# Kernel optimization log

Hardware: AMD Instinct MI355X
Metric: run time of the kernel (lower is better)

Reference implementation:

```python
import jax, jax.numpy as jnp
import numpy as np

DIM = 384
NUM_HEADS = 8
HEAD_DIM = DIM // NUM_HEADS
SCALE = HEAD_DIM ** -0.5
MLP_HIDDEN = int(DIM * 4.0)
EPS = 1e-6


def setup_inputs() -> dict:
    key = jax.random.key(0)
    ks = jax.random.split(key, 8)
    s = 0.02
    return {
        "x": jax.random.normal(ks[0], (2, DIM, 8, 16, 16), dtype=jnp.float32),
        "g1": jnp.ones((DIM,), jnp.float32),
        "b1": jnp.zeros((DIM,), jnp.float32),
        "Wqkv": jax.random.normal(ks[1], (DIM, 3 * DIM), jnp.float32) * s,  # no bias (qkv_bias=False)
        "Wo": jax.random.normal(ks[2], (DIM, DIM), jnp.float32) * s,
        "bo": jnp.zeros((DIM,), jnp.float32),
        "g2": jnp.ones((DIM,), jnp.float32),
        "b2": jnp.zeros((DIM,), jnp.float32),
        "W1": jax.random.normal(ks[3], (DIM, MLP_HIDDEN), jnp.float32) * s,
        "b1m": jnp.zeros((MLP_HIDDEN,), jnp.float32),
        "W2": jax.random.normal(ks[4], (MLP_HIDDEN, DIM), jnp.float32) * s,
        "b2m": jnp.zeros((DIM,), jnp.float32),
    }


def _layernorm(x, g, b):
    mu = jnp.mean(x, axis=-1, keepdims=True)
    var = jnp.mean(jnp.square(x - mu), axis=-1, keepdims=True)
    return (x - mu) * jax.lax.rsqrt(var + EPS) * g + b


def _attention(h, Wqkv, Wo, bo):
    B, N, C = h.shape
    qkv = h @ Wqkv  # [B, N, 3C]
    qkv = qkv.reshape(B, N, 3, NUM_HEADS, HEAD_DIM).transpose(2, 0, 3, 1, 4)
    q, k, v = qkv[0], qkv[1], qkv[2]  # each [B, H, N, d]
    att = jax.nn.softmax(jnp.einsum('bhxd,bhyd->bhxy', q, k) * SCALE, axis=-1)
    out = jnp.einsum('bhxy,bhyd->bhxd', att, v)  # [B, H, N, d]
    out = out.transpose(0, 2, 1, 3).reshape(B, N, C)
    return out @ Wo + bo


def reference(x, g1, b1, Wqkv, Wo, bo, g2, b2, W1, b1m, W2, b2m):
    B, C, D, H, W = x.shape
    h = x.transpose(0, 2, 3, 4, 1).reshape(B, D * H * W, C)  # b (d h w) c
    h = h + _attention(_layernorm(h, g1, b1), Wqkv, Wo, bo)
    m = _layernorm(h, g2, b2)
    m = jax.nn.gelu(m @ W1 + b1m, approximate=False) @ W2 + b2m
    h = h + m
    return h.reshape(B, D, H, W, C).transpose(0, 4, 1, 2, 3)
```

## Files before the change

kernel.cpp:

```cpp
#include <hip/hip_runtime.h>
#include <hip/hip_bf16.h>
#include <math.h>

#define DIM    384
#define NHEAD  8
#define HDIM   48
#define NTOK   2048
#define BATCH  2
#define TOKS   (BATCH * NTOK)
#define HIDDEN 1536

typedef __bf16 bf16x8 __attribute__((ext_vector_type(8)));
typedef float  f32x4  __attribute__((ext_vector_type(4)));
typedef unsigned short u16;

union bfu { __hip_bfloat16 h; u16 u; };

__device__ __forceinline__ void load_lds16(const void* g, void* l) {
    __builtin_amdgcn_global_load_lds(
        (const __attribute__((address_space(1))) void*)g,
        (__attribute__((address_space(3))) void*)l, 16, 0, 0);
}

__global__ __launch_bounds__(256) void prep(
    const float* __restrict__ Wqkv, __hip_bfloat16* __restrict__ WqkvT,
    const float* __restrict__ x, const float* __restrict__ g,
    const float* __restrict__ bta,
    float* __restrict__ hOut, __hip_bfloat16* __restrict__ y) {
    __shared__ __align__(16) char smem[384 * 33 * 4];
    int id = blockIdx.x;
    int tid = threadIdx.x;
    if (id < 432) {
        float (*t)[33] = (float(*)[33])smem;
        const int R = 384, C = 1152, tc = C / 32;
        int i0 = (id / tc) * 32, j0 = (id % tc) * 32;
        int tx = tid & 31, ty = tid >> 5;
#pragma unroll
        for (int k = 0; k < 32; k += 8)
            t[ty + k][tx] = Wqkv[(size_t)(i0 + ty + k) * C + j0 + tx];
        __syncthreads();
#pragma unroll
        for (int k = 0; k < 32; k += 8)
            WqkvT[(size_t)(j0 + ty + k) * R + i0 + tx] = __float2bfloat16(t[tx][ty + k]);
    } else {
        float* t = (float*)smem;
        int id2 = id - 432;
        int n0 = (id2 & 63) * 32, b = id2 >> 6;
        const float* xb = x + (size_t)b * DIM * NTOK;
        for (int idx = tid; idx < 384 * 32; idx += 256) {
            int c = idx >> 5, n = idx & 31;
            t[c * 33 + n] = xb[(size_t)c * NTOK + n0 + n];
        }
        __syncthreads();
        int wid = tid >> 6, lane = tid & 63;
#pragma unroll
        for (int it = 0; it < 8; ++it) {
            int tl = it * 4 + wid;
            float v[6];
            float s = 0.f;
#pragma unroll
            for (int i = 0; i < 6; ++i) { v[i] = t[(lane + 64 * i) * 33 + tl]; s += v[i]; }
#pragma unroll
            for (int o = 32; o; o >>= 1) s += __shfl_xor(s, o, 64);
            float mu = s * (1.f / DIM);
            float s2 = 0.f;
#pragma unroll
            for (int i = 0; i < 6; ++i) { float d = v[i] - mu; s2 += d * d; }
#pragma unroll
            for (int o = 32; o; o >>= 1) s2 += __shfl_xor(s2, o, 64);
            float r = rsqrtf(s2 * (1.f / DIM) + 1e-6f);
            size_t tok = (size_t)b * NTOK + n0 + tl;
#pragma unroll
            for (int i = 0; i < 6; ++i) {
                int c = lane + 64 * i;
                hOut[tok * DIM + c] = v[i];
                y[tok * DIM + c] = __float2bfloat16((v[i] - mu) * r * g[c] + bta[c]);
            }
        }
    }
}

__global__ __launch_bounds__(256) void qkv_gemm_xpose(
    const __hip_bfloat16* __restrict__ A,
    const __hip_bfloat16* __restrict__ BT,
    __hip_bfloat16* __restrict__ Cout,
    __hip_bfloat16* __restrict__ vtout,
    const float* __restrict__ Wo, const float* __restrict__ W1,
    const float* __restrict__ W2,
    __hip_bfloat16* __restrict__ WoT, __hip_bfloat16* __restrict__ W1T,
    __hip_bfloat16* __restrict__ W2T) {
    __shared__ __align__(16) u16 As[2][64 * 32];
    __shared__ __align__(16) u16 Bs[2][64 * 32];
    const int lid = blockIdx.x;
    const int tid = threadIdx.x;
    if (lid < 1152) {
        const int swz = (lid & 7) * 144 + (lid >> 3);
        const int bx = swz % 18, by = swz / 18;
        const int bm = by * 64, bn = bx * 64;
        const int K = DIM;
        int w = tid >> 6, l = tid & 63;
        int m0 = (w >> 1) * 32, n0 = (w & 1) * 32;
        int lm = l & 15, ksel = l >> 4;

        int row = tid >> 2, c16 = tid & 3;
        const __hip_bfloat16* ga = A  + (size_t)(bm + row) * K + c16 * 8;
        const __hip_bfloat16* gb = BT + (size_t)(bn + row) * K + c16 * 8;

        f32x4 acc[2][2] = {};
        for (int k0 = 0; k0 < K; k0 += 64) {
#pragma unroll
            for (int c = 0; c < 2; ++c) {
                load_lds16(ga + k0 + c * 32, &As[c][tid * 8]);
                load_lds16(gb + k0 + c * 32, &Bs[c][tid * 8]);
            }
            __syncthreads();
#pragma unroll
            for (int kk = 0; kk < 2; ++kk) {
                bf16x8 af0 = *(const bf16x8*)&As[kk][(m0 +      lm) * 32 + ksel * 8];
                bf16x8 af1 = *(const bf16x8*)&As[kk][(m0 + 16 + lm) * 32 + ksel * 8];
                bf16x8 bf0 = *(const bf16x8*)&Bs[kk][(n0 +      lm) * 32 + ksel * 8];
                bf16x8 bf1 = *(const bf16x8*)&Bs[kk][(n0 + 16 + lm) * 32 + ksel * 8];
                acc[0][0] = __builtin_amdgcn_mfma_f32_16x16x32_bf16(af0, bf0, acc[0][0], 0, 0, 0);
                acc[0][1] = __builtin_amdgcn_mfma_f32_16x16x32_bf16(af0, bf1, acc[0][1], 0, 0, 0);
                acc[1][0] = __builtin_amdgcn_mfma_f32_16x16x32_bf16(af1, bf0, acc[1][0], 0, 0, 0);
                acc[1][1] = __builtin_amdgcn_mfma_f32_16x16x32_bf16(af1, bf1, acc[1][1], 0, 0, 0);
            }
            __syncthreads();
        }
#pragma unroll
        for (int i = 0; i < 2; ++i)
#pragma unroll
            for (int j = 0; j < 2; ++j)
#pragma unroll
                for (int r = 0; r < 4; ++r) {
                    int rg = bm + m0 + i * 16 + ksel * 4 + r;
                    int cg = bn + n0 + j * 16 + lm;
                    float v = acc[i][j][r];
                    if (cg < 768) {
                        Cout[(size_t)rg * 1152 + cg] = __float2bfloat16(v);
                    } else {
                        int c = cg - 768, hh = c / 48, dd = c - hh * 48;
                        int bb = rg >> 11, n = rg & (NTOK - 1);
                        int kk = n & 127;
                        int pos = ((kk >> 6) << 6) + ((kk & 15) << 2) + ((kk >> 4) & 3);
                        vtout[((size_t)(bb * NHEAD + hh) * 48 + dd) * 2048
                              + (n & ~127) + pos] = __float2bfloat16(v);
                    }
                }
    } else {
        float (*t)[33] = (float(*)[33])As;
        int id = lid - 1152;
        const float* src; __hip_bfloat16* dst; int R, C;
        if (id < 144)      {            src = Wo; dst = WoT; R = 384;  C = 384; }
        else if (id < 720) { id -= 144; src = W1; dst = W1T; R = 384;  C = 1536; }
        else               { id -= 720; src = W2; dst = W2T; R = 1536; C = 384; }
        int tc = C / 32;
        int i0 = (id / tc) * 32, j0 = (id % tc) * 32;
        int tx = tid & 31, ty = tid >> 5;
#pragma unroll
        for (int k = 0; k < 32; k += 8)
            t[ty + k][tx] = src[(size_t)(i0 + ty + k) * C + j0 + tx];
        __syncthreads();
#pragma unroll
        for (int k = 0; k < 32; k += 8)
            dst[(size_t)(j0 + ty + k) * R + i0 + tx] = __float2bfloat16(t[tx][ty + k]);
    }
}

template<int BK, bool GELU, bool BF16OUT, bool TRANSOUT>
__global__ __launch_bounds__(256) void gemm_mfma(
    const __hip_bfloat16* __restrict__ A,
    const __hip_bfloat16* __restrict__ BT,
    const float* __restrict__ bias,
    const float* __restrict__ res,
    void* __restrict__ Cout,
    int M, int N, int K) {
    constexpr int NC = BK / 32;
    __shared__ __align__(16) u16 As[NC][64 * 32];
    __shared__ __align__(16) u16 Bs[NC][64 * 32];
    const int nwg = gridDim.x * gridDim.y;
    const int lid = blockIdx.y * gridDim.x + blockIdx.x;
    const int swz = (lid & 7) * (nwg >> 3) + (lid >> 3);
    const int bx = swz % gridDim.x, by = swz / gridDim.x;
    int bm = by * 64, bn = bx * 64;
    int tid = threadIdx.x;
    int w = tid >> 6, l = tid & 63;
    int m0 = (w >> 1) * 32, n0 = (w & 1) * 32;
    int lm = l & 15, ksel = l >> 4;

    int row = tid >> 2, c16 = tid & 3;
    const __hip_bfloat16* ga = A  + (size_t)(bm + row) * K + c16 * 8;
    const __hip_bfloat16* gb = BT + (size_t)(bn + row) * K + c16 * 8;

    f32x4 acc[2][2] = {};
    for (int k0 = 0; k0 < K; k0 += BK) {
#pragma unroll
        for (int c = 0; c < NC; ++c) {
            load_lds16(ga + k0 + c * 32, &As[c][tid * 8]);
            load_lds16(gb + k0 + c * 32, &Bs[c][tid * 8]);
        }
        __syncthreads();
#pragma unroll
        for (int kk = 0; kk < NC; ++kk) {
            bf16x8 af0 = *(const bf16x8*)&As[kk][(m0 +      lm) * 32 + ksel * 8];
            bf16x8 af1 = *(const bf16x8*)&As[kk][(m0 + 16 + lm) * 32 + ksel * 8];
            bf16x8 bf0 = *(const bf16x8*)&Bs[kk][(n0 +      lm) * 32 + ksel * 8];
            bf16x8 bf1 = *(const bf16x8*)&Bs[kk][(n0 + 16 + lm) * 32 + ksel * 8];
            acc[0][0] = __builtin_amdgcn_mfma_f32_16x16x32_bf16(af0, bf0, acc[0][0], 0, 0, 0);
            acc[0][1] = __builtin_amdgcn_mfma_f32_16x16x32_bf16(af0, bf1, acc[0][1], 0, 0, 0);
            acc[1][0] = __builtin_amdgcn_mfma_f32_16x16x32_bf16(af1, bf0, acc[1][0], 0, 0, 0);
            acc[1][1] = __builtin_amdgcn_mfma_f32_16x16x32_bf16(af1, bf1, acc[1][1], 0, 0, 0);
        }
        __syncthreads();
    }

    if constexpr (TRANSOUT) {
        __shared__ float ct[64 * 65];
#pragma unroll
        for (int i = 0; i < 2; ++i)
#pragma unroll
            for (int j = 0; j < 2; ++j)
#pragma unroll
                for (int r = 0; r < 4; ++r) {
                    int ml = m0 + i * 16 + ksel * 4 + r;
                    int cl = n0 + j * 16 + lm;
                    float v = acc[i][j][r];
                    if (bias) v += bias[bn + cl];
                    if (res)  v += res[(size_t)(bm + ml) * N + bn + cl];
                    ct[ml * 65 + cl] = v;
                }
        __syncthreads();
        int bb = bm >> 11, nb = bm & (NTOK - 1);
        float* outp = (float*)Cout + (size_t)bb * DIM * NTOK + nb;
#pragma unroll
        for (int cl = w; cl < 64; cl += 4)
            outp[(size_t)(bn + cl) * NTOK + l] = ct[l * 65 + cl];
    } else {
#pragma unroll
        for (int i = 0; i < 2; ++i)
#pragma unroll
            for (int j = 0; j < 2; ++j)
#pragma unroll
                for (int r = 0; r < 4; ++r) {
                    int rg = bm + m0 + i * 16 + ksel * 4 + r;
                    int cg = bn + n0 + j * 16 + lm;
                    float v = acc[i][j][r];
                    if (bias) v += bias[cg];
                    if (GELU) v = 0.5f * v * (1.f + erff(v * 0.7071067811865475f));
                    if (res)  v += res[(size_t)rg * N + cg];
                    if constexpr (BF16OUT) {
                        ((__hip_bfloat16*)Cout)[(size_t)rg * N + cg] = __float2bfloat16(v);
                    } else {
                        ((float*)Cout)[(size_t)rg * N + cg] = v;
                    }
                }
    }
}

__global__ __launch_bounds__(256) void wo_ln(
    const __hip_bfloat16* __restrict__ A,
    const __hip_bfloat16* __restrict__ BT,
    const float* __restrict__ bo,
    const float* __restrict__ g2, const float* __restrict__ b2,
    float* __restrict__ h,
    __hip_bfloat16* __restrict__ y) {
    __shared__ __align__(16) u16 As[16 * 64];
    __shared__ __align__(16) u16 Bs[384 * 64];
    __shared__ float red[16 * 8];
    const int r0 = blockIdx.x * 16;
    const int tid = threadIdx.x;
    const int w = tid >> 6, l = tid & 63, lm = l & 15, quad = l >> 4;

    const int arow = tid >> 3;
    const int ag = (tid & 7) ^ (arow & 7);
    const __hip_bfloat16* gaA = A + (size_t)(r0 + arow) * DIM + ag * 8;
    const int xr = lm & 7;

    f32x4 acc[6] = {};
    for (int k0 = 0; k0 < DIM; k0 += 64) {
        if (tid < 128) load_lds16(gaA + k0, (char*)As + tid * 16);
#pragma unroll
        for (int i = 0; i < 12; ++i) {
            int idx = tid + i * 256;
            int brow = idx >> 3;
            int bg = (idx & 7) ^ (brow & 7);
            load_lds16(BT + (size_t)brow * DIM + k0 + bg * 8, (char*)Bs + idx * 16);
        }
        __syncthreads();
#pragma unroll
        for (int kk = 0; kk < 2; ++kk) {
            int goff = ((kk * 4 + quad) ^ xr) * 8;
            bf16x8 af = *(const bf16x8*)&As[lm * 64 + goff];
#pragma unroll
            for (int n = 0; n < 6; ++n) {
                bf16x8 bf = *(const bf16x8*)&Bs[(w * 96 + n * 16 + lm) * 64 + goff];
                acc[n] = __builtin_amdgcn_mfma_f32_16x16x32_bf16(af, bf, acc[n], 0, 0, 0);
            }
        }
        __syncthreads();
    }

    float vv[6][4];
    float s1[4] = {0.f, 0.f, 0.f, 0.f}, s2[4] = {0.f, 0.f, 0.f, 0.f};
#pragma unroll
    for (int r = 0; r < 4; ++r) {
        int rg = r0 + quad * 4 + r;
#pragma unroll
        for (int n = 0; n < 6; ++n) {
            int cg = w * 96 + n * 16 + lm;
            float v = acc[n][r] + bo[cg] + h[(size_t)rg * DIM + cg];
            vv[n][r] = v;
            s1[r] += v;
            s2[r] += v * v;
            h[(size_t)rg * DIM + cg] = v;
        }
    }
#pragma unroll
    for (int r = 0; r < 4; ++r) {
#pragma unroll
        for (int o = 8; o; o >>= 1) {
            s1[r] += __shfl_xor(s1[r], o, 64);
            s2[r] += __shfl_xor(s2[r], o, 64);
        }
        if (lm == 0) {
            red[(quad * 4 + r) * 8 + w * 2]     = s1[r];
            red[(quad * 4 + r) * 8 + w * 2 + 1] = s2[r];
        }
    }
    __syncthreads();
#pragma unroll
    for (int r = 0; r < 4; ++r) {
        int lr = quad * 4 + r;
        float S1 = red[lr * 8] + red[lr * 8 + 2] + red[lr * 8 + 4] + red[lr * 8 + 6];
        float S2 = red[lr * 8 + 1] + red[lr * 8 + 3] + red[lr * 8 + 5] + red[lr * 8 + 7];
        float mu = S1 * (1.f / DIM);
        float var = S2 * (1.f / DIM) - mu * mu;
        float rstd = rsqrtf(var + 1e-6f);
        int rg = r0 + lr;
#pragma unroll
        for (int n = 0; n < 6; ++n) {
            int cg = w * 96 + n * 16 + lm;
            y[(size_t)rg * DIM + cg] =
                __float2bfloat16((vv[n][r] - mu) * rstd * g2[cg] + b2[cg]);
        }
    }
}

#define ATK 128
#define PSTR 136
__global__ __launch_bounds__(512, 4) void attn_mfma(
    const u16* __restrict__ qkv,
    const u16* __restrict__ vt,
    __hip_bfloat16* __restrict__ outp) {
    __shared__ __align__(16) u16 PQ[64 * PSTR];
    __shared__ __align__(16) u16 Ks[128 * 72];
    __shared__ __align__(16) u16 Vs[48 * PSTR];
    const int lid = (blockIdx.z * NHEAD + blockIdx.y) * (NTOK / 64) + blockIdx.x;
    const int swz = (lid & 7) * 64 + (lid >> 3);
    const int q0 = (swz & 31) * 64;
    const int h = (swz >> 5) & 7, b = swz >> 8;
    const int tid = threadIdx.x;
    const int w = tid >> 6, l = tid & 63, lm = l & 15, quad = l >> 4;
    const int qc = w >> 1, kh = w & 1;

    for (int idx = tid; idx < 128; idx += 512) {
        int r = idx >> 1, c = idx & 1;
        *(uint4*)&PQ[r * 72 + 48 + c * 8] = uint4{0, 0, 0, 0};
    }
    for (int idx = tid; idx < 256; idx += 512) {
        int r = idx >> 1, c = idx & 1;
        *(uint4*)&Ks[r * 72 + 48 + c * 8] = uint4{0, 0, 0, 0};
    }
    const u16* qbase = qkv + (size_t)(b * NTOK + q0) * 1152 + h * 48;
    for (int idx = tid; idx < 384; idx += 512) {
        int r = idx / 6, c = idx % 6;
        *(uint4*)&PQ[r * 72 + c * 8] = *(const uint4*)(qbase + (size_t)r * 1152 + c * 8);
    }
    __syncthreads();

    bf16x8 aq0 = *(const bf16x8*)&PQ[(qc * 16 + lm) * 72 +  0 + quad * 8];
    bf16x8 aq1 = *(const bf16x8*)&PQ[(qc * 16 + lm) * 72 + 32 + quad * 8];

    float l_i[4] = {0.f, 0.f, 0.f, 0.f};
    f32x4 o_acc[3] = {};

    const u16* kbase = qkv + (size_t)(b * NTOK) * 1152 + 384 + h * 48;
    const u16* vbase = vt + (size_t)(b * NHEAD + h) * 48 * 2048;
    const float sc2 = 0.14433756729740643f * 1.4426950408889634f;

    const int kr0 = tid / 6,  kc0 = tid % 6;
    const int kr1 = (tid + 512) / 6, kc1 = (tid + 512) % 6;
    const int vd0 = tid >> 4, vc0 = tid & 15;
    const int vd1 = (tid + 512) >> 4, vc1 = (tid + 512) & 15;
    const bool two = tid < 256;
    uint4 kp0, kp1, vp0, vp1;

    {
        kp0 = *(const uint4*)(kbase + (size_t)kr0 * 1152 + kc0 * 8);
        vp0 = *(const uint4*)(vbase + (size_t)vd0 * 2048 + vc0 * 8);
        if (two) {
            kp1 = *(const uint4*)(kbase + (size_t)kr1 * 1152 + kc1 * 8);
            vp1 = *(const uint4*)(vbase + (size_t)vd1 * 2048 + vc1 * 8);
        }
    }

    for (int kt = 0; kt < NTOK / ATK; ++kt) {
        __syncthreads();
        *(uint4*)&Ks[kr0 * 72 + kc0 * 8] = kp0;
        *(uint4*)&Vs[vd0 * PSTR + vc0 * 8] = vp0;
        if (two) {
            *(uint4*)&Ks[kr1 * 72 + kc1 * 8] = kp1;
            *(uint4*)&Vs[vd1 * PSTR + vc1 * 8] = vp1;
        }
        __syncthreads();
        if (kt + 1 < NTOK / ATK) {
            const u16* kb = kbase + (size_t)(kt + 1) * ATK * 1152;
            const u16* vb = vbase + (size_t)(kt + 1) * ATK;
            kp0 = *(const uint4*)(kb + (size_t)kr0 * 1152 + kc0 * 8);
            vp0 = *(const uint4*)(vb + (size_t)vd0 * 2048 + vc0 * 8);
            if (two) {
                kp1 = *(const uint4*)(kb + (size_t)kr1 * 1152 + kc1 * 8);
                vp1 = *(const uint4*)(vb + (size_t)vd1 * 2048 + vc1 * 8);
            }
        }

        f32x4 s[4];
#pragma unroll
        for (int ntp = 0; ntp < 4; ++ntp) {
            int nt = kh * 4 + ntp;
            bf16x8 kf0 = *(const bf16x8*)&Ks[(nt * 16 + lm) * 72 +  0 + quad * 8];
            bf16x8 kf1 = *(const bf16x8*)&Ks[(nt * 16 + lm) * 72 + 32 + quad * 8];
            f32x4 t = {};
            t = __builtin_amdgcn_mfma_f32_16x16x32_bf16(aq0, kf0, t, 0, 0, 0);
            t = __builtin_amdgcn_mfma_f32_16x16x32_bf16(aq1, kf1, t, 0, 0, 0);
            s[ntp] = t;
        }

#pragma unroll
        for (int r = 0; r < 4; ++r) {
            u16 pr[4];
#pragma unroll
            for (int ntp = 0; ntp < 4; ++ntp) {
                float p = exp2f(s[ntp][r] * sc2);
                l_i[r] += p;
                bfu cv; cv.h = __float2bfloat16(p);
                pr[ntp] = cv.u;
            }
            *(uint2*)&PQ[(qc * 16 + quad * 4 + r) * PSTR + kh * 64 + lm * 4] =
                *(const uint2*)pr;
        }

#pragma unroll
        for (int ksp = 0; ksp < 2; ++ksp) {
            int ks = kh * 2 + ksp;
            bf16x8 pf = *(const bf16x8*)&PQ[(qc * 16 + lm) * PSTR + ks * 32 + quad * 8];
#pragma unroll
            for (int nt = 0; nt < 3; ++nt) {
                bf16x8 vf = *(const bf16x8*)&Vs[(nt * 16 + lm) * PSTR + ks * 32 + quad * 8];
                o_acc[nt] = __builtin_amdgcn_mfma_f32_16x16x32_bf16(pf, vf, o_acc[nt], 0, 0, 0);
            }
        }
    }

    __syncthreads();
    float* red = (float*)Ks;
    if (kh == 1) {
        f32x4* base = (f32x4*)&red[(qc * 64 + l) * 16];
        base[0] = o_acc[0]; base[1] = o_acc[1]; base[2] = o_acc[2];
        f32x4 lv; lv[0] = l_i[0]; lv[1] = l_i[1]; lv[2] = l_i[2]; lv[3] = l_i[3];
        base[3] = lv;
    }
    __syncthreads();
    if (kh == 0) {
        f32x4* base = (f32x4*)&red[(qc * 64 + l) * 16];
        o_acc[0] += base[0]; o_acc[1] += base[1]; o_acc[2] += base[2];
        f32x4 lv = base[3];
#pragma unroll
        for (int r = 0; r < 4; ++r) {
            float lsum = l_i[r] + lv[r];
#pragma unroll
            for (int o = 8; o; o >>= 1) lsum += __shfl_xor(lsum, o, 64);
            float inv = 1.f / lsum;
#pragma unroll
            for (int nt = 0; nt < 3; ++nt)
                outp[(size_t)(b * NTOK + q0 + qc * 16 + quad * 4 + r) * DIM
                     + h * 48 + nt * 16 + lm]
                    = __float2bfloat16(o_acc[nt][r] * inv);
        }
    }
}

extern "C" void kernel_launch(void* const* d_in, const int* in_sizes, int n_in,
                              void* d_out, int out_size, void* d_ws, size_t ws_size,
                              hipStream_t stream) {
    const float* x    = (const float*)d_in[0];
    const float* g1   = (const float*)d_in[1];
    const float* b1   = (const float*)d_in[2];
    const float* Wqkv = (const float*)d_in[3];
    const float* Wo   = (const float*)d_in[4];
    const float* bo   = (const float*)d_in[5];
    const float* g2   = (const float*)d_in[6];
    const float* b2   = (const float*)d_in[7];
    const float* W1   = (const float*)d_in[8];
    const float* b1m  = (const float*)d_in[9];
    const float* W2   = (const float*)d_in[10];
    const float* b2m  = (const float*)d_in[11];
    float* out = (float*)d_out;

    char* p = (char*)d_ws;
    float* bufH = (float*)p;                       p += (size_t)TOKS * DIM * 4;
    char* qkvp = p;
    __hip_bfloat16* bufQKVb = (__hip_bfloat16*)p;  p += (size_t)TOKS * 3 * DIM * 2;
    __hip_bfloat16* bufVT   = (__hip_bfloat16*)p;  p += (size_t)TOKS * DIM * 2;
    __hip_bfloat16* bufNb   = (__hip_bfloat16*)p;  p += (size_t)TOKS * DIM * 2;
    __hip_bfloat16* bufAb   = (__hip_bfloat16*)p;  p += (size_t)TOKS * DIM * 2;
    __hip_bfloat16* WqkvT   = (__hip_bfloat16*)p;  p += (size_t)3 * DIM * DIM * 2;
    __hip_bfloat16* WoT     = (__hip_bfloat16*)p;  p += (size_t)DIM * DIM * 2;
    __hip_bfloat16* W1T     = (__hip_bfloat16*)p;  p += (size_t)HIDDEN * DIM * 2;
    __hip_bfloat16* W2T     = (__hip_bfloat16*)p;  p += (size_t)DIM * HIDDEN * 2;
    __hip_bfloat16* bufHIDb = (__hip_bfloat16*)qkvp;

    prep<<<432 + 128, 256, 0, stream>>>(Wqkv, WqkvT, x, g1, b1, bufH, bufNb);
    qkv_gemm_xpose<<<1152 + 1296, 256, 0, stream>>>(
        bufNb, WqkvT, bufQKVb, bufVT, Wo, W1, W2, WoT, W1T, W2T);
    attn_mfma<<<dim3(NTOK / 64, NHEAD, BATCH), 512, 0, stream>>>(
        (const u16*)bufQKVb, (const u16*)bufVT, bufAb);
    wo_ln<<<TOKS / 16, 256, 0, stream>>>(bufAb, WoT, bo, g2, b2, bufH, bufNb);
    gemm_mfma<64, true, true, false><<<dim3(HIDDEN / 64, TOKS / 64), 256, 0, stream>>>(
        bufNb, W1T, b1m, nullptr, bufHIDb, TOKS, HIDDEN, DIM);
    gemm_mfma<128, false, false, true><<<dim3(DIM / 64, TOKS / 64), 256, 0, stream>>>(
        bufHIDb, W2T, b2m, bufH, out, TOKS, DIM, HIDDEN);
}
```

Measured before the change: 186.4 us.

## Add dedicated W2 GEMM kernel with smaller M tiles and swizzled LDS

Replaces the generic transposed-output GEMM used for the W2 projection with a dedicated kernel. It uses 32x64 output tiles so the grid doubles from 384 to 768 workgroups, and a K-step of 128 held in an XOR-swizzled LDS layout to reduce bank conflicts on fragment loads. The generic GEMM template is simplified to the bf16 GELU path only. Each workgroup now reloads the full B tile for half as many output rows, so per-output B traffic rises, and each wave issues fewer MFMAs per LDS load.

```diff
diff --git a/kernel.cpp b/kernel.cpp
--- a/kernel.cpp
+++ b/kernel.cpp
@@ -167,13 +167,12 @@
     }
 }
 
-template<int BK, bool GELU, bool BF16OUT, bool TRANSOUT>
+template<int BK, bool GELU>
 __global__ __launch_bounds__(256) void gemm_mfma(
     const __hip_bfloat16* __restrict__ A,
     const __hip_bfloat16* __restrict__ BT,
     const float* __restrict__ bias,
-    const float* __restrict__ res,
-    void* __restrict__ Cout,
+    __hip_bfloat16* __restrict__ Cout,
     int M, int N, int K) {
     constexpr int NC = BK / 32;
     __shared__ __align__(16) u16 As[NC][64 * 32];
@@ -214,46 +213,88 @@
         __syncthreads();
     }
 
-    if constexpr (TRANSOUT) {
-        __shared__ float ct[64 * 65];
-#pragma unroll
-        for (int i = 0; i < 2; ++i)
-#pragma unroll
-            for (int j = 0; j < 2; ++j)
-#pragma unroll
-                for (int r = 0; r < 4; ++r) {
-                    int ml = m0 + i * 16 + ksel * 4 + r;
-                    int cl = n0 + j * 16 + lm;
-                    float v = acc[i][j][r];
-                    if (bias) v += bias[bn + cl];
-                    if (res)  v += res[(size_t)(bm + ml) * N + bn + cl];
-                    ct[ml * 65 + cl] = v;
-                }
-        __syncthreads();
-        int bb = bm >> 11, nb = bm & (NTOK - 1);
-        float* outp = (float*)Cout + (size_t)bb * DIM * NTOK + nb;
-#pragma unroll
-        for (int cl = w; cl < 64; cl += 4)
-            outp[(size_t)(bn + cl) * NTOK + l] = ct[l * 65 + cl];
-    } else {
-#pragma unroll
-        for (int i = 0; i < 2; ++i)
-#pragma unroll
-            for (int j = 0; j < 2; ++j)
-#pragma unroll
-                for (int r = 0; r < 4; ++r) {
-                    int rg = bm + m0 + i * 16 + ksel * 4 + r;
-                    int cg = bn + n0 + j * 16 + lm;
-                    float v = acc[i][j][r];
-                    if (bias) v += bias[cg];
-                    if (GELU) v = 0.5f * v * (1.f + erff(v * 0.7071067811865475f));
-                    if (res)  v += res[(size_t)rg * N + cg];
-                    if constexpr (BF16OUT) {
-                        ((__hip_bfloat16*)Cout)[(size_t)rg * N + cg] = __float2bfloat16(v);
-                    } else {
-                        ((float*)Cout)[(size_t)rg * N + cg] = v;
-                    }
-                }
+#pragma unroll
+    for (int i = 0; i < 2; ++i)
+#pragma unroll
+        for (int j = 0; j < 2; ++j)
+#pragma unroll
+            for (int r = 0; r < 4; ++r) {
+                int rg = bm + m0 + i * 16 + ksel * 4 + r;
+                int cg = bn + n0 + j * 16 + lm;
+                float v = acc[i][j][r];
+                if (bias) v += bias[cg];
+                if (GELU) v = 0.5f * v * (1.f + erff(v * 0.7071067811865475f));
+                Cout[(size_t)rg * N + cg] = __float2bfloat16(v);
+            }
+}
+
+__global__ __launch_bounds__(256) void w2_gemm(
+    const __hip_bfloat16* __restrict__ A,
+    const __hip_bfloat16* __restrict__ BT,
+    const float* __restrict__ bias,
+    const float* __restrict__ res,
+    float* __restrict__ outp) {
+    __shared__ __align__(16) u16 As[32 * 128];
+    __shared__ __align__(16) u16 Bs[64 * 128];
+    __shared__ float ct[32 * 65];
+    const int K = HIDDEN, N = DIM;
+    const int nwg = gridDim.x * gridDim.y;
+    const int lid = blockIdx.y * gridDim.x + blockIdx.x;
+    const int swz = (lid & 7) * (nwg >> 3) + (lid >> 3);
+    const int bx = swz % gridDim.x, by = swz / gridDim.x;
+    const int bm = by * 32, bn = bx * 64;
+    const int tid = threadIdx.x;
+    const int w = tid >> 6, l = tid & 63;
+    const int n0 = w * 16;
+    const int lm = l & 15, ksel = l >> 4;
+    const int xr = lm & 7;
+
+    f32x4 acc[2] = {};
+    for (int k0 = 0; k0 < K; k0 += 128) {
+#pragma unroll
+        for (int i = 0; i < 2; ++i) {
+            int idx = tid + i * 256;
+            int row = idx >> 4, p = idx & 15;
+            int g = p ^ (row & 7);
+            load_lds16(A + (size_t)(bm + row) * K + k0 + g * 8, (char*)As + idx * 16);
+        }
+#pragma unroll
+        for (int i = 0; i < 4; ++i) {
+            int idx = tid + i * 256;
+            int row = idx >> 4, p = idx & 15;
+            int g = p ^ (row & 7);
+            load_lds16(BT + (size_t)(bn + row) * K + k0 + g * 8, (char*)Bs + idx * 16);
+        }
+        __syncthreads();
+#pragma unroll
+        for (int kk = 0; kk < 4; ++kk) {
+            int gq = ((kk * 4 + ksel) ^ xr) * 8;
+            bf16x8 af0 = *(const bf16x8*)&As[lm        * 128 + gq];
+            bf16x8 af1 = *(const bf16x8*)&As[(16 + lm) * 128 + gq];
+            bf16x8 bf  = *(const bf16x8*)&Bs[(n0 + lm) * 128 + gq];
+            acc[0] = __builtin_amdgcn_mfma_f32_16x16x32_bf16(af0, bf, acc[0], 0, 0, 0);
+            acc[1] = __builtin_amdgcn_mfma_f32_16x16x32_bf16(af1, bf, acc[1], 0, 0, 0);
+        }
+        __syncthreads();
+    }
+
+#pragma unroll
+    for (int m = 0; m < 2; ++m)
+#pragma unroll
+        for (int r = 0; r < 4; ++r) {
+            int ml = m * 16 + ksel * 4 + r;
+            int cl = n0 + lm;
+            float v = acc[m][r] + bias[bn + cl]
+                    + res[(size_t)(bm + ml) * N + bn + cl];
+            ct[ml * 65 + cl] = v;
+        }
+    __syncthreads();
+    int bb = bm >> 11, nb = bm & (NTOK - 1);
+    float* op = outp + (size_t)bb * DIM * NTOK + nb;
+#pragma unroll
+    for (int cc = w * 2; cc < 64; cc += 8) {
+        int cl = cc + (l >> 5), rw = l & 31;
+        op[(size_t)(bn + cl) * NTOK + rw] = ct[rw * 65 + cl];
     }
 }
 
@@ -526,8 +567,8 @@
     attn_mfma<<<dim3(NTOK / 64, NHEAD, BATCH), 512, 0, stream>>>(
         (const u16*)bufQKVb, (const u16*)bufVT, bufAb);
     wo_ln<<<TOKS / 16, 256, 0, stream>>>(bufAb, WoT, bo, g2, b2, bufH, bufNb);
-    gemm_mfma<64, true, true, false><<<dim3(HIDDEN / 64, TOKS / 64), 256, 0, stream>>>(
-        bufNb, W1T, b1m, nullptr, bufHIDb, TOKS, HIDDEN, DIM);
-    gemm_mfma<128, false, false, true><<<dim3(DIM / 64, TOKS / 64), 256, 0, stream>>>(
-        bufHIDb, W2T, b2m, bufH, out, TOKS, DIM, HIDDEN);
-}
+    gemm_mfma<64, true><<<dim3(HIDDEN / 64, TOKS / 64), 256, 0, stream>>>(
+        bufNb, W1T, b1m, bufHIDb, TOKS, HIDDEN, DIM);
+    w2_gemm<<<dim3(DIM / 64, TOKS / 32), 256, 0, stream>>>(
+        bufHIDb, W2T, b2m, bufH, out);
+}
```

Result: faster. 179.6 us, median of 2 (-3.6%).
